# Optimization experiments

Measured on AMD Instinct MI355X. Metric: run time of the kernel, lower is better.

## Reference

```python
import jax, jax.numpy as jnp
import numpy as np

N = 100000   # nodes
E = 3200000  # edges
C = 256      # in_channels
H = 64       # hidden_channels
G = 512      # graphs in batch
FC = [128, 64, 32, 16]
OUT = 2
EPS = 1e-5


def _linear(key, fan_in, fan_out):
    k1, k2 = jax.random.split(key)
    s = 1.0 / np.sqrt(fan_in)
    W = jax.random.uniform(k1, (fan_in, fan_out), jnp.float32, -s, s)
    b = jax.random.uniform(k2, (fan_out,), jnp.float32, -s, s)
    return W, b


def setup_inputs() -> dict:
    key = jax.random.key(0)
    ks = jax.random.split(key, 12)
    x = jax.random.normal(ks[0], (N, C), jnp.float32)
    edge_index = jax.random.randint(ks[1], (2, E), 0, N, dtype=jnp.int64)
    batch = jnp.sort(jax.random.randint(ks[2], (N,), 0, G, dtype=jnp.int64))
    w1, b1 = _linear(ks[3], C, H)
    w2, b2 = _linear(ks[4], H, H)
    g1 = jnp.ones((H,), jnp.float32); be1 = jnp.zeros((H,), jnp.float32)
    g2 = jnp.ones((H,), jnp.float32); be2 = jnp.zeros((H,), jnp.float32)
    fw1, fb1 = _linear(ks[5], H, FC[0])
    fw2, fb2 = _linear(ks[6], FC[0], FC[1])
    fw3, fb3 = _linear(ks[7], FC[1], FC[2])
    fw4, fb4 = _linear(ks[8], FC[2], FC[3])
    ow, ob = _linear(ks[9], FC[3], OUT)
    return dict(x=x, edge_index=edge_index, batch=batch,
                w1=w1, b1=b1, w2=w2, b2=b2,
                g1=g1, be1=be1, g2=g2, be2=be2,
                fw1=fw1, fb1=fb1, fw2=fw2, fb2=fb2,
                fw3=fw3, fb3=fb3, fw4=fw4, fb4=fb4,
                ow=ow, ob=ob)


def _gcn_layers(x, edge_index, w1, b1, w2, b2, g1, be1, g2, be2):
    # PyG GCNConv: add self loops, symmetric deg^-1/2 normalization, scatter-add at dst
    loops = jnp.arange(N, dtype=edge_index.dtype)
    src = jnp.concatenate([edge_index[0], loops])
    dst = jnp.concatenate([edge_index[1], loops])
    deg = jax.ops.segment_sum(jnp.ones((E + N,), jnp.float32), dst, num_segments=N)
    dis = jnp.where(deg > 0, jax.lax.rsqrt(jnp.maximum(deg, 1.0)), 0.0)
    norm = (dis[src] * dis[dst])[:, None]  # [E+N, 1]

    def conv(h, W, b):
        h = h @ W
        return jax.ops.segment_sum(h[src] * norm, dst, num_segments=N) + b

    def bn(h, g, be):  # BatchNorm1d over node dim (training-mode batch stats)
        m = jnp.mean(h, axis=0)
        v = jnp.var(h, axis=0)
        return (h - m) * jax.lax.rsqrt(v + EPS) * g + be

    h = bn(jax.nn.relu(conv(x, w1, b1)), g1, be1)   # dropout = identity (eval)
    h = bn(jax.nn.relu(conv(h, w2, b2)), g2, be2)
    return h


def reference(x, edge_index, batch, w1, b1, w2, b2, g1, be1, g2, be2,
              fw1, fb1, fw2, fb2, fw3, fb3, fw4, fb4, ow, ob):
    h = _gcn_layers(x, edge_index, w1, b1, w2, b2, g1, be1, g2, be2)
    # global_mean_pool over batch vector
    s = jax.ops.segment_sum(h, batch, num_segments=G)
    cnt = jax.ops.segment_sum(jnp.ones((N,), jnp.float32), batch, num_segments=G)
    p = s / jnp.maximum(cnt, 1.0)[:, None]  # [G, H]
    h = jax.nn.relu(p @ fw1 + fb1)
    h = jax.nn.relu(h @ fw2 + fb2)
    h = jax.nn.relu(h @ fw3 + fb3)
    h = jax.nn.relu(h @ fw4 + fb4)
    return h @ ow + ob  # [G, OUT]
```

## Files before the change

### kernel.cpp

```cpp
#include <hip/hip_runtime.h>
#include <hip/hip_fp16.h>

#define N_NODES 100000
#define E_EDGES 3200000
#define NG      512
#define BN_EPS  1e-5f

#define BSH     7
#define BNODES  128
#define NBUCK   782
#define NCHUNK  200
#define CHUNK   16000

__global__ __launch_bounds__(256) void k_zero(float* __restrict__ stats1,
                                              float* __restrict__ stats2,
                                              float* __restrict__ sums,
                                              float* __restrict__ cnt) {
  int i = blockIdx.x * 256 + threadIdx.x;
  if (i < 128) { stats1[i] = 0.f; stats2[i] = 0.f; }
  if (i < NG * 64) sums[i] = 0.f;
  if (i < NG) cnt[i] = 0.f;
}

__global__ __launch_bounds__(256) void kb_hist(const int* __restrict__ ei,
                                               int* __restrict__ counts) {
  __shared__ int h[NBUCK];
  const int c = blockIdx.x, tid = threadIdx.x;
  for (int b = tid; b < NBUCK; b += 256) h[b] = 0;
  __syncthreads();
  const int* dst = ei + E_EDGES + c * CHUNK;
  for (int i = tid; i < CHUNK; i += 256) atomicAdd(&h[dst[i] >> BSH], 1);
  __syncthreads();
  for (int b = tid; b < NBUCK; b += 256) counts[b * NCHUNK + c] = h[b];
}

__global__ __launch_bounds__(256) void kb_scan1(int* __restrict__ counts,
                                                int* __restrict__ btot) {
  __shared__ int sm[256];
  const int b = blockIdx.x, tid = threadIdx.x;
  const int cval = (tid < NCHUNK) ? counts[b * NCHUNK + tid] : 0;
  int val = cval;
  sm[tid] = val;
  __syncthreads();
  for (int off = 1; off < 256; off <<= 1) {
    int t = (tid >= off) ? sm[tid - off] : 0;
    __syncthreads();
    val += t;
    sm[tid] = val;
    __syncthreads();
  }
  if (tid < NCHUNK) counts[b * NCHUNK + tid] = val - cval;
  if (tid == 255) btot[b] = val;
}

__global__ __launch_bounds__(1024) void kb_scan2(const int* __restrict__ btot,
                                                 int* __restrict__ bbase) {
  __shared__ int sm[1024];
  const int tid = threadIdx.x;
  const int cval = (tid < NBUCK) ? btot[tid] : 0;
  int val = cval;
  sm[tid] = val;
  __syncthreads();
  for (int off = 1; off < 1024; off <<= 1) {
    int t = (tid >= off) ? sm[tid - off] : 0;
    __syncthreads();
    val += t;
    sm[tid] = val;
    __syncthreads();
  }
  if (tid < NBUCK) bbase[tid] = val - cval;
  if (tid == NBUCK - 1) bbase[NBUCK] = val;
}

__global__ __launch_bounds__(256) void kb_scatter(const int* __restrict__ ei,
                                                  const int* __restrict__ counts,
                                                  const int* __restrict__ bbase,
                                                  int* __restrict__ binned) {
  __shared__ int cur[NBUCK];
  const int c = blockIdx.x, tid = threadIdx.x;
  for (int b = tid; b < NBUCK; b += 256) cur[b] = bbase[b] + counts[b * NCHUNK + c];
  __syncthreads();
  const int* srcp = ei + c * CHUNK;
  const int* dstp = ei + E_EDGES + c * CHUNK;
  for (int i = tid; i < CHUNK; i += 256) {
    const int s = srcp[i], d = dstp[i];
    const int pos = atomicAdd(&cur[d >> BSH], 1);
    binned[pos] = ((d & (BNODES - 1)) << 17) | s;
  }
}

__global__ __launch_bounds__(256) void kb_degsort(const int* __restrict__ binned,
                                                  const int* __restrict__ bbase,
                                                  int* __restrict__ csr,
                                                  int* __restrict__ row_start,
                                                  float* __restrict__ dis) {
  __shared__ int h[BNODES];
  __shared__ int pre[BNODES];
  const int b = blockIdx.x, tid = threadIdx.x;
  if (tid < BNODES) h[tid] = 0;
  __syncthreads();
  const int e0 = bbase[b], e1 = bbase[b + 1];
  for (int i = e0 + tid; i < e1; i += 256) atomicAdd(&h[binned[i] >> 17], 1);
  __syncthreads();
  if (tid < BNODES) pre[tid] = h[tid];
  __syncthreads();
  for (int off = 1; off < BNODES; off <<= 1) {
    int t = (tid >= off && tid < BNODES) ? pre[tid - off] : 0;
    __syncthreads();
    if (tid < BNODES) pre[tid] += t;
    __syncthreads();
  }
  if (tid < BNODES) {
    const int n = b * BNODES + tid;
    const int ex = e0 + pre[tid] - h[tid];
    if (n < N_NODES) {
      row_start[n] = ex;
      dis[n] = rsqrtf((float)(h[tid] + 1));
    }
    h[tid] = ex;
  }
  if (b == NBUCK - 1 && tid == 0) row_start[N_NODES] = E_EDGES;
  __syncthreads();
  for (int i = e0 + tid; i < e1; i += 256) {
    const int v = binned[i];
    const int pos = atomicAdd(&h[v >> 17], 1);
    csr[pos] = v & 0x1FFFF;
  }
}

template <int K, bool BN>
__global__ __launch_bounds__(256) void k_gemm(const float* __restrict__ in,
                                              const float* __restrict__ W,
                                              const float* __restrict__ dis,
                                              const float* __restrict__ stats,
                                              const float* __restrict__ gam,
                                              const float* __restrict__ bet,
                                              __half* __restrict__ y) {
  __shared__ float xs[64 * 68];
  __shared__ float wsm[64 * 64];
  __shared__ float scv[64], shv[64];
  const int tid = threadIdx.x;
  const int n0 = blockIdx.x * 64;
  const int lane = tid & 63, wv = tid >> 6;
  const int nq = lane & 15;
  const int chb = wv * 16 + (lane >> 4) * 4;
  if (BN) {
    if (tid < 64) {
      const float m = stats[tid] * (1.0f / N_NODES);
      const float v = stats[64 + tid] * (1.0f / N_NODES) - m * m;
      const float sc = rsqrtf(v + BN_EPS) * gam[tid];
      scv[tid] = sc;
      shv[tid] = bet[tid] - m * sc;
    }
  }
  float a[4][4] = {{0,0,0,0},{0,0,0,0},{0,0,0,0},{0,0,0,0}};
  for (int c0 = 0; c0 < K; c0 += 64) {
    __syncthreads();
#pragma unroll
    for (int i = 0; i < 4; ++i) {
      const int idx = tid + i * 256;
      const int n = idx >> 4, c4 = (idx & 15) * 4;
      const int nn = min(n0 + n, N_NODES - 1);
      float4 v = *(const float4*)&in[(size_t)nn * K + c0 + c4];
      if (BN) {
        v.x = v.x * scv[c4] + shv[c4];
        v.y = v.y * scv[c4 + 1] + shv[c4 + 1];
        v.z = v.z * scv[c4 + 2] + shv[c4 + 2];
        v.w = v.w * scv[c4 + 3] + shv[c4 + 3];
      }
      *(float4*)&xs[n * 68 + c4] = v;
    }
#pragma unroll
    for (int i = 0; i < 4; ++i) {
      const int idx = tid + i * 256;
      const int c = idx >> 4, ch4 = (idx & 15) * 4;
      *(float4*)&wsm[c * 64 + ch4] = *(const float4*)&W[(size_t)(c0 + c) * 64 + ch4];
    }
    __syncthreads();
    for (int c = 0; c < 64; c += 4) {
      float wq[4][4];
#pragma unroll
      for (int cc = 0; cc < 4; ++cc) {
        const float4 w4 = *(const float4*)&wsm[(c + cc) * 64 + chb];
        wq[cc][0] = w4.x; wq[cc][1] = w4.y; wq[cc][2] = w4.z; wq[cc][3] = w4.w;
      }
#pragma unroll
      for (int i = 0; i < 4; ++i) {
        const float4 xv = *(const float4*)&xs[(nq + 16 * i) * 68 + c];
#pragma unroll
        for (int j = 0; j < 4; ++j) {
          a[i][j] = fmaf(xv.x, wq[0][j],
                    fmaf(xv.y, wq[1][j],
                    fmaf(xv.z, wq[2][j],
                    fmaf(xv.w, wq[3][j], a[i][j]))));
        }
      }
    }
  }
#pragma unroll
  for (int i = 0; i < 4; ++i) {
    const int n = n0 + nq + 16 * i;
    if (n < N_NODES) {
      const float d = dis[n];
      union { __half h[4]; float2 f; } u;
      u.h[0] = __float2half_rn(d * a[i][0]);
      u.h[1] = __float2half_rn(d * a[i][1]);
      u.h[2] = __float2half_rn(d * a[i][2]);
      u.h[3] = __float2half_rn(d * a[i][3]);
      *(float2*)&y[(size_t)n * 64 + chb] = u.f;
    }
  }
}

__global__ __launch_bounds__(256) void k_gather(const int* __restrict__ csr,
                                                const int* __restrict__ rs,
                                                const __half* __restrict__ y,
                                                const float* __restrict__ dis,
                                                const float* __restrict__ bias,
                                                float* __restrict__ hout,
                                                float* __restrict__ stats) {
  const int tid = threadIdx.x;
  const int lane = tid & 63;
  const int wid = (blockIdx.x * 256 + tid) >> 6;
  const int nw = (gridDim.x * 256) >> 6;
  const int per = (N_NODES + nw - 1) / nw;
  const int n0 = wid * per;
  const int n1 = min(N_NODES, n0 + per);
  const float b = bias[lane];
  float s1 = 0.f, s2 = 0.f;
  for (int n = n0; n < n1; ++n) {
    int e = rs[n];
    const int end = rs[n + 1];
    float a = __half2float(y[(size_t)n * 64 + lane]);
    float a2 = 0.f;
    for (; e + 4 <= end; e += 4) {
      const int i0 = csr[e], i1 = csr[e + 1], i2 = csr[e + 2], i3 = csr[e + 3];
      const float v0 = __half2float(y[(size_t)i0 * 64 + lane]);
      const float v1 = __half2float(y[(size_t)i1 * 64 + lane]);
      const float v2 = __half2float(y[(size_t)i2 * 64 + lane]);
      const float v3 = __half2float(y[(size_t)i3 * 64 + lane]);
      a += v0 + v1;
      a2 += v2 + v3;
    }
    for (; e < end; ++e) a += __half2float(y[(size_t)csr[e] * 64 + lane]);
    float v = fmaxf(dis[n] * (a + a2) + b, 0.f);
    hout[(size_t)n * 64 + lane] = v;
    s1 += v;
    s2 += v * v;
  }
  __shared__ float r1[256], r2[256];
  r1[tid] = s1;
  r2[tid] = s2;
  __syncthreads();
  if (tid < 64) {
    atomicAdd(&stats[tid], r1[tid] + r1[tid + 64] + r1[tid + 128] + r1[tid + 192]);
  } else if (tid < 128) {
    const int h = tid - 64;
    atomicAdd(&stats[64 + h], r2[h] + r2[h + 64] + r2[h + 128] + r2[h + 192]);
  }
}

__global__ __launch_bounds__(256) void k_pool(const float* __restrict__ hin,
                                              const float* __restrict__ stats,
                                              const float* __restrict__ gam,
                                              const float* __restrict__ bet,
                                              const int* __restrict__ batch,
                                              float* __restrict__ sums,
                                              float* __restrict__ cnt) {
  const int lane = threadIdx.x & 63;
  const int wid = (blockIdx.x * 256 + threadIdx.x) >> 6;
  const int nw = (gridDim.x * 256) >> 6;
  const int per = (N_NODES + nw - 1) / nw;
  const int n0 = wid * per;
  const int n1 = min(N_NODES, n0 + per);
  const float m = stats[lane] * (1.0f / N_NODES);
  const float v = stats[64 + lane] * (1.0f / N_NODES) - m * m;
  const float sc = rsqrtf(v + BN_EPS) * gam[lane];
  const float sh = bet[lane] - m * sc;
  int cur = -1, run = 0;
  float a = 0.f;
  for (int n = n0; n < n1; ++n) {
    const int b = batch[n];
    if (b != cur) {
      if (run) {
        atomicAdd(&sums[cur * 64 + lane], a);
        if (lane == 0) atomicAdd(&cnt[cur], (float)run);
      }
      cur = b; run = 0; a = 0.f;
    }
    a += hin[(size_t)n * 64 + lane] * sc + sh;
    ++run;
  }
  if (run) {
    atomicAdd(&sums[cur * 64 + lane], a);
    if (lane == 0) atomicAdd(&cnt[cur], (float)run);
  }
}

__global__ __launch_bounds__(128) void k_mlp(const float* __restrict__ sums,
                                             const float* __restrict__ cnt,
                                             const float* __restrict__ fw1, const float* __restrict__ fb1,
                                             const float* __restrict__ fw2, const float* __restrict__ fb2,
                                             const float* __restrict__ fw3, const float* __restrict__ fb3,
                                             const float* __restrict__ fw4, const float* __restrict__ fb4,
                                             const float* __restrict__ ow, const float* __restrict__ ob,
                                             float* __restrict__ out) {
  __shared__ float u0[128], u1[128];
  const int g = blockIdx.x, t = threadIdx.x;
  if (t < 64) u0[t] = sums[g * 64 + t] / fmaxf(cnt[g], 1.0f);
  __syncthreads();
  if (t < 128) {
    float a = fb1[t];
    for (int k = 0; k < 64; ++k) a = fmaf(u0[k], fw1[k * 128 + t], a);
    u1[t] = fmaxf(a, 0.f);
  }
  __syncthreads();
  if (t < 64) {
    float a = fb2[t];
    for (int k = 0; k < 128; ++k) a = fmaf(u1[k], fw2[k * 64 + t], a);
    u0[t] = fmaxf(a, 0.f);
  }
  __syncthreads();
  if (t < 32) {
    float a = fb3[t];
    for (int k = 0; k < 64; ++k) a = fmaf(u0[k], fw3[k * 32 + t], a);
    u1[t] = fmaxf(a, 0.f);
  }
  __syncthreads();
  if (t < 16) {
    float a = fb4[t];
    for (int k = 0; k < 32; ++k) a = fmaf(u1[k], fw4[k * 16 + t], a);
    u0[t] = fmaxf(a, 0.f);
  }
  __syncthreads();
  if (t < 2) {
    float a = ob[t];
    for (int k = 0; k < 16; ++k) a = fmaf(u0[k], ow[k * 2 + t], a);
    out[g * 2 + t] = a;
  }
}

extern "C" void kernel_launch(void* const* d_in, const int* in_sizes, int n_in,
                              void* d_out, int out_size, void* d_ws, size_t ws_size,
                              hipStream_t stream) {
  const float* x    = (const float*)d_in[0];
  const int*   ei   = (const int*)d_in[1];
  const int*   batch= (const int*)d_in[2];
  const float* w1   = (const float*)d_in[3];
  const float* b1   = (const float*)d_in[4];
  const float* w2   = (const float*)d_in[5];
  const float* b2   = (const float*)d_in[6];
  const float* g1   = (const float*)d_in[7];
  const float* be1  = (const float*)d_in[8];
  const float* g2   = (const float*)d_in[9];
  const float* be2  = (const float*)d_in[10];
  const float* fw1  = (const float*)d_in[11]; const float* fb1 = (const float*)d_in[12];
  const float* fw2  = (const float*)d_in[13]; const float* fb2 = (const float*)d_in[14];
  const float* fw3  = (const float*)d_in[15]; const float* fb3 = (const float*)d_in[16];
  const float* fw4  = (const float*)d_in[17]; const float* fb4 = (const float*)d_in[18];
  const float* ow   = (const float*)d_in[19]; const float* ob  = (const float*)d_in[20];
  float* out = (float*)d_out;

  char* ws = (char*)d_ws;
  auto alloc = [&](size_t bytes) {
    void* p = ws;
    ws += (bytes + 255) & ~(size_t)255;
    return p;
  };
  float*  dis      = (float*)alloc((size_t)N_NODES * 4);
  int*    counts   = (int*)  alloc((size_t)NBUCK * NCHUNK * 4);
  int*    btot     = (int*)  alloc((size_t)NBUCK * 4);
  int*    bbase    = (int*)  alloc((size_t)(NBUCK + 1) * 4);
  int*    binned   = (int*)  alloc((size_t)E_EDGES * 4);
  int*    csr      = (int*)  alloc((size_t)E_EDGES * 4);
  int*    row_start= (int*)  alloc((size_t)(N_NODES + 1) * 4);
  __half* yH       = (__half*)alloc((size_t)N_NODES * 64 * 2);
  float*  hB       = (float*)alloc((size_t)N_NODES * 64 * 4);
  float*  stats1   = (float*)alloc(512);
  float*  stats2   = (float*)alloc(512);
  float*  sums     = (float*)alloc((size_t)NG * 64 * 4);
  float*  cnt      = (float*)alloc((size_t)NG * 4);

  const int nblkG = (N_NODES + 63) / 64;

  k_zero    <<<128, 256, 0, stream>>>(stats1, stats2, sums, cnt);
  kb_hist   <<<NCHUNK, 256, 0, stream>>>(ei, counts);
  kb_scan1  <<<NBUCK, 256, 0, stream>>>(counts, btot);
  kb_scan2  <<<1, 1024, 0, stream>>>(btot, bbase);
  kb_scatter<<<NCHUNK, 256, 0, stream>>>(ei, counts, bbase, binned);
  kb_degsort<<<NBUCK, 256, 0, stream>>>(binned, bbase, csr, row_start, dis);

  k_gemm<256, false><<<nblkG, 256, 0, stream>>>(x, w1, dis, nullptr, nullptr, nullptr, yH);
  k_gather<<<2048, 256, 0, stream>>>(csr, row_start, yH, dis, b1, hB, stats1);

  k_gemm<64, true><<<nblkG, 256, 0, stream>>>(hB, w2, dis, stats1, g1, be1, yH);
  k_gather<<<2048, 256, 0, stream>>>(csr, row_start, yH, dis, b2, hB, stats2);

  k_pool<<<512, 256, 0, stream>>>(hB, stats2, g2, be2, batch, sums, cnt);
  k_mlp <<<NG, 128, 0, stream>>>(sums, cnt, fw1, fb1, fw2, fb2, fw3, fb3, fw4, fb4, ow, ob, out);
}
```

Before: 680.4 us.

## Fuse mean-pool into second gather, vectorize half2 gather, widen edge binning chunks

The second aggregation kernel now accumulates per-graph sums and counts directly, so the separate pooling kernel and the write and re-read of the N×64 float hidden buffer go away. BatchNorm2 is applied after pooling inside the MLP kernel, which is valid because BN is affine and the mean commutes with it. The gather loop now reads half2 values, with the two wave halves processing alternate edges and combining through a shuffle. The binning histogram uses 1024 chunks instead of 200 for more parallelism, and the scan runs with 1024 threads. The cost is more atomics into the per-graph sums and half the lanes sitting idle in the epilogue.

Result: faster. 601.9 us (-11.5%).

```diff
diff --git a/kernel.cpp b/kernel.cpp
--- a/kernel.cpp
+++ b/kernel.cpp
@@ -9,8 +9,8 @@
 #define BSH     7
 #define BNODES  128
 #define NBUCK   782
-#define NCHUNK  200
-#define CHUNK   16000
+#define NCHUNK  1024
+#define CHUNK   3125
 
 __global__ __launch_bounds__(256) void k_zero(float* __restrict__ stats1,
                                               float* __restrict__ stats2,
@@ -34,23 +34,23 @@
   for (int b = tid; b < NBUCK; b += 256) counts[b * NCHUNK + c] = h[b];
 }
 
-__global__ __launch_bounds__(256) void kb_scan1(int* __restrict__ counts,
-                                                int* __restrict__ btot) {
-  __shared__ int sm[256];
+__global__ __launch_bounds__(1024) void kb_scan1(int* __restrict__ counts,
+                                                 int* __restrict__ btot) {
+  __shared__ int sm[NCHUNK];
   const int b = blockIdx.x, tid = threadIdx.x;
-  const int cval = (tid < NCHUNK) ? counts[b * NCHUNK + tid] : 0;
+  const int cval = counts[b * NCHUNK + tid];
   int val = cval;
   sm[tid] = val;
   __syncthreads();
-  for (int off = 1; off < 256; off <<= 1) {
+  for (int off = 1; off < NCHUNK; off <<= 1) {
     int t = (tid >= off) ? sm[tid - off] : 0;
     __syncthreads();
     val += t;
     sm[tid] = val;
     __syncthreads();
   }
-  if (tid < NCHUNK) counts[b * NCHUNK + tid] = val - cval;
-  if (tid == 255) btot[b] = val;
+  counts[b * NCHUNK + tid] = val - cval;
+  if (tid == NCHUNK - 1) btot[b] = val;
 }
 
 __global__ __launch_bounds__(1024) void kb_scan2(const int* __restrict__ btot,
@@ -212,45 +212,99 @@
   }
 }
 
+template <bool POOL>
 __global__ __launch_bounds__(256) void k_gather(const int* __restrict__ csr,
                                                 const int* __restrict__ rs,
                                                 const __half* __restrict__ y,
                                                 const float* __restrict__ dis,
                                                 const float* __restrict__ bias,
                                                 float* __restrict__ hout,
-                                                float* __restrict__ stats) {
+                                                float* __restrict__ stats,
+                                                const int* __restrict__ batch,
+                                                float* __restrict__ sums,
+                                                float* __restrict__ cnt) {
   const int tid = threadIdx.x;
   const int lane = tid & 63;
+  const int p = lane >> 5;
+  const int c = lane & 31;
   const int wid = (blockIdx.x * 256 + tid) >> 6;
   const int nw = (gridDim.x * 256) >> 6;
   const int per = (N_NODES + nw - 1) / nw;
   const int n0 = wid * per;
   const int n1 = min(N_NODES, n0 + per);
-  const float b = bias[lane];
-  float s1 = 0.f, s2 = 0.f;
+  const float bx = bias[2 * c], by = bias[2 * c + 1];
+  float s1x = 0.f, s1y = 0.f, s2x = 0.f, s2y = 0.f;
+  int curg = -1, run = 0;
+  float px = 0.f, py = 0.f;
   for (int n = n0; n < n1; ++n) {
     int e = rs[n];
     const int end = rs[n + 1];
-    float a = __half2float(y[(size_t)n * 64 + lane]);
-    float a2 = 0.f;
-    for (; e + 4 <= end; e += 4) {
-      const int i0 = csr[e], i1 = csr[e + 1], i2 = csr[e + 2], i3 = csr[e + 3];
-      const float v0 = __half2float(y[(size_t)i0 * 64 + lane]);
-      const float v1 = __half2float(y[(size_t)i1 * 64 + lane]);
-      const float v2 = __half2float(y[(size_t)i2 * 64 + lane]);
-      const float v3 = __half2float(y[(size_t)i3 * 64 + lane]);
-      a += v0 + v1;
-      a2 += v2 + v3;
-    }
-    for (; e < end; ++e) a += __half2float(y[(size_t)csr[e] * 64 + lane]);
-    float v = fmaxf(dis[n] * (a + a2) + b, 0.f);
-    hout[(size_t)n * 64 + lane] = v;
-    s1 += v;
-    s2 += v * v;
+    float ax = 0.f, ay = 0.f;
+    if (p == 0) {
+      const float2 f = __half22float2(*(const __half2*)&y[(size_t)n * 64 + 2 * c]);
+      ax = f.x; ay = f.y;
+    }
+    for (; e + 8 <= end; e += 8) {
+      const int i0 = csr[e + p];
+      const int i1 = csr[e + 2 + p];
+      const int i2 = csr[e + 4 + p];
+      const int i3 = csr[e + 6 + p];
+      const float2 f0 = __half22float2(*(const __half2*)&y[(size_t)i0 * 64 + 2 * c]);
+      const float2 f1 = __half22float2(*(const __half2*)&y[(size_t)i1 * 64 + 2 * c]);
+      const float2 f2 = __half22float2(*(const __half2*)&y[(size_t)i2 * 64 + 2 * c]);
+      const float2 f3 = __half22float2(*(const __half2*)&y[(size_t)i3 * 64 + 2 * c]);
+      ax += (f0.x + f1.x) + (f2.x + f3.x);
+      ay += (f0.y + f1.y) + (f2.y + f3.y);
+    }
+    for (; e + 2 <= end; e += 2) {
+      const int i0 = csr[e + p];
+      const float2 f = __half22float2(*(const __half2*)&y[(size_t)i0 * 64 + 2 * c]);
+      ax += f.x; ay += f.y;
+    }
+    if (e < end && p == 0) {
+      const int i0 = csr[e];
+      const float2 f = __half22float2(*(const __half2*)&y[(size_t)i0 * 64 + 2 * c]);
+      ax += f.x; ay += f.y;
+    }
+    ax += __shfl_xor(ax, 32);
+    ay += __shfl_xor(ay, 32);
+    const float d = dis[n];
+    const float vx = fmaxf(d * ax + bx, 0.f);
+    const float vy = fmaxf(d * ay + by, 0.f);
+    if (lane < 32) {
+      if (!POOL) *(float2*)&hout[(size_t)n * 64 + 2 * c] = make_float2(vx, vy);
+      s1x += vx; s1y += vy;
+      s2x += vx * vx; s2y += vy * vy;
+    }
+    if (POOL) {
+      const int g = batch[n];
+      if (g != curg) {
+        if (run) {
+          if (lane < 32) {
+            atomicAdd(&sums[curg * 64 + 2 * c], px);
+            atomicAdd(&sums[curg * 64 + 2 * c + 1], py);
+          }
+          if (lane == 0) atomicAdd(&cnt[curg], (float)run);
+        }
+        curg = g; run = 0; px = 0.f; py = 0.f;
+      }
+      if (lane < 32) { px += vx; py += vy; }
+      ++run;
+    }
+  }
+  if (POOL && run) {
+    if (lane < 32) {
+      atomicAdd(&sums[curg * 64 + 2 * c], px);
+      atomicAdd(&sums[curg * 64 + 2 * c + 1], py);
+    }
+    if (lane == 0) atomicAdd(&cnt[curg], (float)run);
   }
   __shared__ float r1[256], r2[256];
-  r1[tid] = s1;
-  r2[tid] = s2;
+  const int wv = tid >> 6;
+  if (lane < 32) {
+    r1[wv * 64 + 2 * c] = s1x; r1[wv * 64 + 2 * c + 1] = s1y;
+    r2[wv * 64 + 2 * c] = s2x; r2[wv * 64 + 2 * c + 1] = s2y;
+  }
   __syncthreads();
   if (tid < 64) {
     atomicAdd(&stats[tid], r1[tid] + r1[tid + 64] + r1[tid + 128] + r1[tid + 192]);
@@ -260,45 +314,11 @@
   }
 }
 
-__global__ __launch_bounds__(256) void k_pool(const float* __restrict__ hin,
-                                              const float* __restrict__ stats,
-                                              const float* __restrict__ gam,
-                                              const float* __restrict__ bet,
-                                              const int* __restrict__ batch,
-                                              float* __restrict__ sums,
-                                              float* __restrict__ cnt) {
-  const int lane = threadIdx.x & 63;
-  const int wid = (blockIdx.x * 256 + threadIdx.x) >> 6;
-  const int nw = (gridDim.x * 256) >> 6;
-  const int per = (N_NODES + nw - 1) / nw;
-  const int n0 = wid * per;
-  const int n1 = min(N_NODES, n0 + per);
-  const float m = stats[lane] * (1.0f / N_NODES);
-  const float v = stats[64 + lane] * (1.0f / N_NODES) - m * m;
-  const float sc = rsqrtf(v + BN_EPS) * gam[lane];
-  const float sh = bet[lane] - m * sc;
-  int cur = -1, run = 0;
-  float a = 0.f;
-  for (int n = n0; n < n1; ++n) {
-    const int b = batch[n];
-    if (b != cur) {
-      if (run) {
-        atomicAdd(&sums[cur * 64 + lane], a);
-        if (lane == 0) atomicAdd(&cnt[cur], (float)run);
-      }
-      cur = b; run = 0; a = 0.f;
-    }
-    a += hin[(size_t)n * 64 + lane] * sc + sh;
-    ++run;
-  }
-  if (run) {
-    atomicAdd(&sums[cur * 64 + lane], a);
-    if (lane == 0) atomicAdd(&cnt[cur], (float)run);
-  }
-}
-
 __global__ __launch_bounds__(128) void k_mlp(const float* __restrict__ sums,
                                              const float* __restrict__ cnt,
+                                             const float* __restrict__ stats,
+                                             const float* __restrict__ gam,
+                                             const float* __restrict__ bet,
                                              const float* __restrict__ fw1, const float* __restrict__ fb1,
                                              const float* __restrict__ fw2, const float* __restrict__ fb2,
                                              const float* __restrict__ fw3, const float* __restrict__ fb3,
@@ -307,7 +327,13 @@
                                              float* __restrict__ out) {
   __shared__ float u0[128], u1[128];
   const int g = blockIdx.x, t = threadIdx.x;
-  if (t < 64) u0[t] = sums[g * 64 + t] / fmaxf(cnt[g], 1.0f);
+  if (t < 64) {
+    const float m = stats[t] * (1.0f / N_NODES);
+    const float v = stats[64 + t] * (1.0f / N_NODES) - m * m;
+    const float sc = rsqrtf(v + BN_EPS) * gam[t];
+    const float sh = bet[t] - m * sc;
+    u0[t] = (sums[g * 64 + t] / fmaxf(cnt[g], 1.0f)) * sc + sh;
+  }
   __syncthreads();
   if (t < 128) {
     float a = fb1[t];
@@ -385,17 +411,19 @@
 
   k_zero    <<<128, 256, 0, stream>>>(stats1, stats2, sums, cnt);
   kb_hist   <<<NCHUNK, 256, 0, stream>>>(ei, counts);
-  kb_scan1  <<<NBUCK, 256, 0, stream>>>(counts, btot);
+  kb_scan1  <<<NBUCK, NCHUNK, 0, stream>>>(counts, btot);
   kb_scan2  <<<1, 1024, 0, stream>>>(btot, bbase);
   kb_scatter<<<NCHUNK, 256, 0, stream>>>(ei, counts, bbase, binned);
   kb_degsort<<<NBUCK, 256, 0, stream>>>(binned, bbase, csr, row_start, dis);
 
   k_gemm<256, false><<<nblkG, 256, 0, stream>>>(x, w1, dis, nullptr, nullptr, nullptr, yH);
-  k_gather<<<2048, 256, 0, stream>>>(csr, row_start, yH, dis, b1, hB, stats1);
+  k_gather<false><<<2048, 256, 0, stream>>>(csr, row_start, yH, dis, b1, hB, stats1,
+                                            nullptr, nullptr, nullptr);
 
   k_gemm<64, true><<<nblkG, 256, 0, stream>>>(hB, w2, dis, stats1, g1, be1, yH);
-  k_gather<<<2048, 256, 0, stream>>>(csr, row_start, yH, dis, b2, hB, stats2);
-
-  k_pool<<<512, 256, 0, stream>>>(hB, stats2, g2, be2, batch, sums, cnt);
-  k_mlp <<<NG, 128, 0, stream>>>(sums, cnt, fw1, fb1, fw2, fb2, fw3, fb3, fw4, fb4, ow, ob, out);
-}
+  k_gather<true><<<2048, 256, 0, stream>>>(csr, row_start, yH, dis, b2, nullptr, stats2,
+                                           batch, sums, cnt);
+
+  k_mlp<<<NG, 128, 0, stream>>>(sums, cnt, stats2, g2, be2,
+                                fw1, fb1, fw2, fb2, fw3, fb3, fw4, fb4, ow, ob, out);
+}
```
